# Performance work log

Hardware: AMD Instinct MI355X
Metric: run time of the kernel (lower is better)

Reference implementation:

```python
import jax, jax.numpy as jnp
import numpy as np

N = 50000
E = 800000
D_IN = 128
H = 256
L = 3


def setup_inputs() -> dict:
    key = jax.random.key(0)
    ks = jax.random.split(key, 12)
    x = jax.random.normal(ks[0], (N, D_IN), dtype=jnp.float32)
    edge_index = jax.random.randint(ks[1], (2, E), 0, N, dtype=jnp.int32)
    edge_attr = jax.random.uniform(ks[2], (E, 4), dtype=jnp.float32)
    s_enc = 1.0 / np.sqrt(D_IN)
    s_h = 1.0 / np.sqrt(H)
    W_enc = jax.random.uniform(ks[3], (D_IN, H), minval=-s_enc, maxval=s_enc)
    b_enc = jax.random.uniform(ks[4], (H,), minval=-s_enc, maxval=s_enc)
    W_g = jax.random.uniform(ks[5], (L, H, H), minval=-s_h, maxval=s_h)
    b_g = jax.random.uniform(ks[6], (L, H), minval=-s_h, maxval=s_h)
    W_out = jax.random.uniform(ks[7], (H, H), minval=-s_h, maxval=s_h)
    b_out = jax.random.uniform(ks[8], (H,), minval=-s_h, maxval=s_h)
    return {"x": x, "edge_index": edge_index, "edge_attr": edge_attr,
            "W_enc": W_enc, "b_enc": b_enc, "W_g": W_g, "b_g": b_g,
            "W_out": W_out, "b_out": b_out}


def _gcn_norm(edge_index, n):
    # PyG GCNConv: add self-loops, symmetric normalization D^-1/2 (A+I) D^-1/2
    loops = jnp.arange(n, dtype=edge_index.dtype)
    src = jnp.concatenate([edge_index[0], loops])  # [E+N]
    dst = jnp.concatenate([edge_index[1], loops])  # [E+N]
    deg = jax.ops.segment_sum(jnp.ones_like(dst, dtype=jnp.float32), dst, num_segments=n)
    dinv = jnp.where(deg > 0, jax.lax.rsqrt(deg), 0.0)
    norm = dinv[src] * dinv[dst]  # [E+N]
    return src, dst, norm


def _gcn_conv(h, W, b, src, dst, norm, n):
    m = h @ W                                  # [N,H] transform first
    agg = jax.ops.segment_sum(m[src] * norm[:, None], dst, num_segments=n)
    return agg + b


def reference(x, edge_index, edge_attr, W_enc, b_enc, W_g, b_g, W_out, b_out):
    n = x.shape[0]
    src, dst, norm = _gcn_norm(edge_index, n)
    h = jax.nn.relu(x @ W_enc + b_enc)
    for i in range(W_g.shape[0]):
        h = jax.nn.relu(_gcn_conv(h, W_g[i], b_g[i], src, dst, norm, n))
        # dropout is identity in eval mode
    return h @ W_out + b_out
```

## Files before the change

kernel.cpp:

```cpp
#include <hip/hip_runtime.h>
#include <math.h>

#define N_NODES 50000
#define N_EDGES 800000
#define D_IN    128
#define H_DIM   256
#define L_LAYERS 3
#define SCAN_BLOCKS ((N_NODES + 255) / 256)

typedef _Float16 f16x8 __attribute__((ext_vector_type(8)));
typedef _Float16 f16x4 __attribute__((ext_vector_type(4)));
typedef float    f32x4 __attribute__((ext_vector_type(4)));


__global__ __launch_bounds__(256) void zero_kernel(int* __restrict__ counts,
                                                   int* __restrict__ cursor, int n) {
    int i = blockIdx.x * 256 + threadIdx.x;
    if (i < n) { counts[i] = 0; cursor[i] = 0; }
}

__global__ __launch_bounds__(256) void hist_kernel(const int* __restrict__ dst,
                                                   int* __restrict__ counts, int e_cnt) {
    int e = blockIdx.x * 256 + threadIdx.x;
    if (e < e_cnt) atomicAdd(&counts[dst[e]], 1);
}

__global__ __launch_bounds__(256) void scanA_kernel(const int* __restrict__ counts,
                                                    int* __restrict__ blocksum,
                                                    float* __restrict__ dinv, int n) {
    __shared__ int s[256];
    int t = threadIdx.x;
    int i = blockIdx.x * 256 + t;
    int v = (i < n) ? counts[i] : 0;
    if (i < n) dinv[i] = rsqrtf((float)(v + 1));
    s[t] = v;
    __syncthreads();
#pragma unroll
    for (int d = 128; d > 0; d >>= 1) {
        if (t < d) s[t] += s[t + d];
        __syncthreads();
    }
    if (t == 0) blocksum[blockIdx.x] = s[0];
}

__global__ __launch_bounds__(256) void scanB_kernel(int* __restrict__ blocksum,
                                                    int* __restrict__ offsets,
                                                    int nblocks, int n, int total) {
    __shared__ int s[256];
    int t = threadIdx.x;
    int v = (t < nblocks) ? blocksum[t] : 0;
    s[t] = v;
    __syncthreads();
#pragma unroll
    for (int d = 1; d < 256; d <<= 1) {
        int x = (t >= d) ? s[t - d] : 0;
        __syncthreads();
        s[t] += x;
        __syncthreads();
    }
    if (t < nblocks) blocksum[t] = s[t] - v;
    if (t == 0) offsets[n] = total;
}

__global__ __launch_bounds__(256) void scanC_kernel(const int* __restrict__ counts,
                                                    const int* __restrict__ blocksum,
                                                    int* __restrict__ offsets, int n) {
    __shared__ int s[256];
    int t = threadIdx.x;
    int i = blockIdx.x * 256 + t;
    int v = (i < n) ? counts[i] : 0;
    s[t] = v;
    __syncthreads();
#pragma unroll
    for (int d = 1; d < 256; d <<= 1) {
        int x = (t >= d) ? s[t - d] : 0;
        __syncthreads();
        s[t] += x;
        __syncthreads();
    }
    if (i < n) offsets[i] = blocksum[blockIdx.x] + s[t] - v;
}

__global__ __launch_bounds__(256) void fill_kernel(const int* __restrict__ src,
                                                   const int* __restrict__ dst,
                                                   const int* __restrict__ offsets,
                                                   int* __restrict__ cursor,
                                                   const float* __restrict__ dinv,
                                                   int* __restrict__ csr_src,
                                                   float* __restrict__ csr_w, int e_cnt) {
    int e = blockIdx.x * 256 + threadIdx.x;
    if (e < e_cnt) {
        int d = dst[e];
        int pos = offsets[d] + atomicAdd(&cursor[d], 1);
        int s = src[e];
        csr_src[pos] = s;
        csr_w[pos]   = dinv[s];
    }
}


__global__ __launch_bounds__(256) void aggregate_kernel(const _Float16* __restrict__ h,
                                                        const int* __restrict__ offsets,
                                                        const int* __restrict__ csr_src,
                                                        const float* __restrict__ csr_w,
                                                        const float* __restrict__ dinv,
                                                        _Float16* __restrict__ outp, int n) {
    int wave = threadIdx.x >> 6;
    int lane = threadIdx.x & 63;
    int v = blockIdx.x * 4 + wave;
    if (v >= n) return;
    int c = lane * 4;
    float dv = dinv[v];
    f16x4 self = *(const f16x4*)(h + (size_t)v * H_DIM + c);
    float ax = dv * (float)self[0];
    float ay = dv * (float)self[1];
    float az = dv * (float)self[2];
    float aw = dv * (float)self[3];

    int e  = offsets[v];
    int e1 = offsets[v + 1];
    for (; e + 3 < e1; e += 4) {
        int   s0 = csr_src[e],     s1 = csr_src[e + 1];
        int   s2 = csr_src[e + 2], s3 = csr_src[e + 3];
        float w0 = csr_w[e],       w1 = csr_w[e + 1];
        float w2 = csr_w[e + 2],   w3 = csr_w[e + 3];
        f16x4 a = *(const f16x4*)(h + (size_t)s0 * H_DIM + c);
        f16x4 b = *(const f16x4*)(h + (size_t)s1 * H_DIM + c);
        f16x4 d = *(const f16x4*)(h + (size_t)s2 * H_DIM + c);
        f16x4 f = *(const f16x4*)(h + (size_t)s3 * H_DIM + c);
        ax += w0 * (float)a[0] + w1 * (float)b[0] + w2 * (float)d[0] + w3 * (float)f[0];
        ay += w0 * (float)a[1] + w1 * (float)b[1] + w2 * (float)d[1] + w3 * (float)f[1];
        az += w0 * (float)a[2] + w1 * (float)b[2] + w2 * (float)d[2] + w3 * (float)f[2];
        aw += w0 * (float)a[3] + w1 * (float)b[3] + w2 * (float)d[3] + w3 * (float)f[3];
    }
    for (; e < e1; ++e) {
        int   s0 = csr_src[e];
        float w0 = csr_w[e];
        f16x4 a = *(const f16x4*)(h + (size_t)s0 * H_DIM + c);
        ax += w0 * (float)a[0]; ay += w0 * (float)a[1];
        az += w0 * (float)a[2]; aw += w0 * (float)a[3];
    }
    f16x4 o;
    o[0] = (_Float16)(ax * dv);
    o[1] = (_Float16)(ay * dv);
    o[2] = (_Float16)(az * dv);
    o[3] = (_Float16)(aw * dv);
    *(f16x4*)(outp + (size_t)v * H_DIM + c) = o;
}


#define WCONV_TOTAL 294912

__global__ __launch_bounds__(256) void wconv_kernel(const float* __restrict__ W_enc,
                                                    const float* __restrict__ W_g,
                                                    const float* __restrict__ W_out,
                                                    _Float16* __restrict__ whi,
                                                    _Float16* __restrict__ wlo) {
    int gid = blockIdx.x * 256 + threadIdx.x;
    if (gid >= WCONV_TOTAL) return;
    const float* src; int base, e;
    if (gid < 32768)       { src = W_enc; base = 0;      e = gid; }
    else if (gid < 229376) { src = W_g;   base = 32768;  e = gid - 32768; }
    else                   { src = W_out; base = 229376; e = gid - 229376; }
    int k = e >> 8;
    int n = e & 255;
    float x = src[e];
    _Float16 hb = (_Float16)x;
    _Float16 lb = (_Float16)(x - (float)hb);
    int dst = base + (k >> 5) * 8192 + (n >> 4) * 512 + ((k & 31) >> 3) * 128
            + (n & 15) * 8 + (k & 7);
    whi[dst] = hb;
    wlo[dst] = lb;
}


template <int AMODE, int OUT16>
__global__ __launch_bounds__(256, 3) void mfma_gemm(const float* __restrict__ Af,
                                                    const _Float16* __restrict__ A16,
                                                    int K,
                                                    const _Float16* __restrict__ WhG,
                                                    const _Float16* __restrict__ WlG,
                                                    const float* __restrict__ bias,
                                                    float* __restrict__ Cf,
                                                    _Float16* __restrict__ Ch,
                                                    int n, int relu) {
    __shared__ _Float16 Wh[8192];
    __shared__ _Float16 Wl[8192];

    int t = threadIdx.x;
    int w = t >> 6;
    int lane = t & 63;
    int row0 = blockIdx.x * 64;
    int mrow = lane & 15;
    int koct = (lane >> 4) * 8;

    f32x4 acc[4][4];
#pragma unroll
    for (int mt = 0; mt < 4; ++mt)
#pragma unroll
        for (int c = 0; c < 4; ++c)
            acc[mt][c] = (f32x4)(0.0f);

    int rows[4];
#pragma unroll
    for (int mt = 0; mt < 4; ++mt) {
        int r = row0 + mt * 16 + mrow;
        rows[mt] = (r < n) ? r : (n - 1);
    }

    int nkc = K >> 5;
    for (int kc = 0; kc < nkc; ++kc) {
        {
            const _Float16* gh = WhG + (size_t)kc * 8192;
            const _Float16* gl = WlG + (size_t)kc * 8192;
#pragma unroll
            for (int i = 0; i < 4; ++i) {
                int chunk = w * 4 + i;
                __builtin_amdgcn_global_load_lds(
                    (const __attribute__((address_space(1))) unsigned int*)(gh + chunk * 512 + lane * 8),
                    (__attribute__((address_space(3))) unsigned int*)(&Wh[chunk * 512]),
                    16, 0, 0);
                __builtin_amdgcn_global_load_lds(
                    (const __attribute__((address_space(1))) unsigned int*)(gl + chunk * 512 + lane * 8),
                    (__attribute__((address_space(3))) unsigned int*)(&Wl[chunk * 512]),
                    16, 0, 0);
            }
        }

        f16x8 ahf[4], alf[4];
        if (AMODE == 1) {
#pragma unroll
            for (int mt = 0; mt < 4; ++mt)
                ahf[mt] = *(const f16x8*)(A16 + (size_t)rows[mt] * K + kc * 32 + koct);
        } else {
#pragma unroll
            for (int mt = 0; mt < 4; ++mt) {
                const float* p = Af + (size_t)rows[mt] * K + kc * 32 + koct;
                float4 a0 = *(const float4*)p;
                float4 a1 = *(const float4*)(p + 4);
                float xs[8] = {a0.x, a0.y, a0.z, a0.w, a1.x, a1.y, a1.z, a1.w};
                f16x8 H, L;
#pragma unroll
                for (int j = 0; j < 8; ++j) {
                    _Float16 hb = (_Float16)xs[j];
                    H[j] = hb;
                    L[j] = (_Float16)(xs[j] - (float)hb);
                }
                ahf[mt] = H;
                alf[mt] = L;
            }
        }
        __syncthreads();

#pragma unroll
        for (int c = 0; c < 4; ++c) {
            int nt = w * 4 + c;
            f16x8 bh = *(const f16x8*)&Wh[(nt * 64 + lane) * 8];
            f16x8 bl = *(const f16x8*)&Wl[(nt * 64 + lane) * 8];
#pragma unroll
            for (int mt = 0; mt < 4; ++mt) {
                acc[mt][c] = __builtin_amdgcn_mfma_f32_16x16x32_f16(ahf[mt], bh, acc[mt][c], 0, 0, 0);
                acc[mt][c] = __builtin_amdgcn_mfma_f32_16x16x32_f16(ahf[mt], bl, acc[mt][c], 0, 0, 0);
                if (AMODE == 0)
                    acc[mt][c] = __builtin_amdgcn_mfma_f32_16x16x32_f16(alf[mt], bh, acc[mt][c], 0, 0, 0);
            }
        }
        __syncthreads();
    }

    int colq = lane & 15;
    int rowq = (lane >> 4) * 4;
#pragma unroll
    for (int c = 0; c < 4; ++c) {
        int col = w * 64 + c * 16 + colq;
        float b = bias[col];
#pragma unroll
        for (int mt = 0; mt < 4; ++mt) {
            int rb = row0 + mt * 16 + rowq;
#pragma unroll
            for (int r = 0; r < 4; ++r) {
                int row = rb + r;
                if (row < n) {
                    float v = acc[mt][c][r] + b;
                    if (relu) v = fmaxf(v, 0.f);
                    if (OUT16) Ch[(size_t)row * H_DIM + col] = (_Float16)v;
                    else       Cf[(size_t)row * H_DIM + col] = v;
                }
            }
        }
    }
}


extern "C" void kernel_launch(void* const* d_in, const int* in_sizes, int n_in,
                              void* d_out, int out_size, void* d_ws, size_t ws_size,
                              hipStream_t stream) {
    const float* x     = (const float*)d_in[0];
    const int*   ei    = (const int*)d_in[1];
    const float* W_enc = (const float*)d_in[3];
    const float* b_enc = (const float*)d_in[4];
    const float* W_g   = (const float*)d_in[5];
    const float* b_g   = (const float*)d_in[6];
    const float* W_out = (const float*)d_in[7];
    const float* b_out = (const float*)d_in[8];
    float* out = (float*)d_out;

    char* ws = (char*)d_ws;
    size_t off = 0;
    auto alloc = [&](size_t bytes) -> void* {
        void* p = ws + off;
        off = (off + bytes + 255) & ~(size_t)255;
        return p;
    };
    int*       counts   = (int*)alloc((size_t)N_NODES * 4);
    int*       offsets  = (int*)alloc((size_t)(N_NODES + 1) * 4);
    int*       cursor   = (int*)alloc((size_t)N_NODES * 4);
    float*     dinv     = (float*)alloc((size_t)N_NODES * 4);
    int*       blocksum = (int*)alloc((size_t)SCAN_BLOCKS * 4);
    int*       csr_src  = (int*)alloc((size_t)N_EDGES * 4);
    float*     csr_w    = (float*)alloc((size_t)N_EDGES * 4);
    _Float16*  h16      = (_Float16*)alloc((size_t)N_NODES * H_DIM * 2);
    _Float16*  agg16    = (_Float16*)alloc((size_t)N_NODES * H_DIM * 2);
    _Float16*  whi      = (_Float16*)alloc((size_t)WCONV_TOTAL * 2);
    _Float16*  wlo      = (_Float16*)alloc((size_t)WCONV_TOTAL * 2);

    const int* src = ei;
    const int* dst = ei + N_EDGES;

    zero_kernel<<<(N_NODES + 255) / 256, 256, 0, stream>>>(counts, cursor, N_NODES);
    hist_kernel<<<(N_EDGES + 255) / 256, 256, 0, stream>>>(dst, counts, N_EDGES);
    scanA_kernel<<<SCAN_BLOCKS, 256, 0, stream>>>(counts, blocksum, dinv, N_NODES);
    scanB_kernel<<<1, 256, 0, stream>>>(blocksum, offsets, SCAN_BLOCKS, N_NODES, N_EDGES);
    scanC_kernel<<<SCAN_BLOCKS, 256, 0, stream>>>(counts, blocksum, offsets, N_NODES);
    fill_kernel<<<(N_EDGES + 255) / 256, 256, 0, stream>>>(src, dst, offsets, cursor, dinv,
                                                           csr_src, csr_w, N_EDGES);
    wconv_kernel<<<(WCONV_TOTAL + 255) / 256, 256, 0, stream>>>(W_enc, W_g, W_out, whi, wlo);

    int gemm_grid = (N_NODES + 63) / 64;
    mfma_gemm<0, 1><<<gemm_grid, 256, 0, stream>>>(x, (const _Float16*)nullptr, D_IN,
                                                   whi, wlo, b_enc,
                                                   (float*)nullptr, h16, N_NODES, 1);
    for (int l = 0; l < L_LAYERS; ++l) {
        aggregate_kernel<<<N_NODES / 4, 256, 0, stream>>>(h16, offsets, csr_src, csr_w, dinv,
                                                          agg16, N_NODES);
        mfma_gemm<1, 1><<<gemm_grid, 256, 0, stream>>>((const float*)nullptr, agg16, H_DIM,
                                                       whi + 32768 + (size_t)l * 65536,
                                                       wlo + 32768 + (size_t)l * 65536,
                                                       b_g + (size_t)l * H_DIM,
                                                       (float*)nullptr, h16, N_NODES, 1);
    }
    mfma_gemm<1, 0><<<gemm_grid, 256, 0, stream>>>((const float*)nullptr, h16, H_DIM,
                                                   whi + 229376, wlo + 229376, b_out,
                                                   out, (_Float16*)nullptr, N_NODES, 0);
}
```

Baseline: 563.7 us.

## Make GEMM persistent with resident weight column slices and software-prefetched A tiles

The GEMM becomes a persistent kernel of 512 blocks. Each block loads a 64-column slice of the full-K weights into LDS once, then loops over 256-row tiles, prefetching the next K-chunk of A into registers while the current one runs through MFMA. This removes the per-K-chunk weight reloads and barriers and hides A load latency, at the cost of lower occupancy (launch bounds 2) and extra register pressure. The aggregation loop is also widened to batch 8 neighbor gathers per iteration, giving more memory-level parallelism.

```diff
diff --git a/kernel.cpp b/kernel.cpp
--- a/kernel.cpp
+++ b/kernel.cpp
@@ -119,21 +119,48 @@
 
     int e  = offsets[v];
     int e1 = offsets[v + 1];
-    for (; e + 3 < e1; e += 4) {
-        int   s0 = csr_src[e],     s1 = csr_src[e + 1];
-        int   s2 = csr_src[e + 2], s3 = csr_src[e + 3];
-        float w0 = csr_w[e],       w1 = csr_w[e + 1];
-        float w2 = csr_w[e + 2],   w3 = csr_w[e + 3];
+
+    for (; e + 7 < e1; e += 8) {
+        int   s_[8]; float w_[8]; f16x4 r_[8];
+#pragma unroll
+        for (int j = 0; j < 8; ++j) { s_[j] = csr_src[e + j]; w_[j] = csr_w[e + j]; }
+#pragma unroll
+        for (int j = 0; j < 8; ++j) r_[j] = *(const f16x4*)(h + (size_t)s_[j] * H_DIM + c);
+#pragma unroll
+        for (int j = 0; j < 8; ++j) {
+            ax += w_[j] * (float)r_[j][0];
+            ay += w_[j] * (float)r_[j][1];
+            az += w_[j] * (float)r_[j][2];
+            aw += w_[j] * (float)r_[j][3];
+        }
+    }
+    if (e + 3 < e1) {
+        int   s_[4]; float w_[4]; f16x4 r_[4];
+#pragma unroll
+        for (int j = 0; j < 4; ++j) { s_[j] = csr_src[e + j]; w_[j] = csr_w[e + j]; }
+#pragma unroll
+        for (int j = 0; j < 4; ++j) r_[j] = *(const f16x4*)(h + (size_t)s_[j] * H_DIM + c);
+#pragma unroll
+        for (int j = 0; j < 4; ++j) {
+            ax += w_[j] * (float)r_[j][0];
+            ay += w_[j] * (float)r_[j][1];
+            az += w_[j] * (float)r_[j][2];
+            aw += w_[j] * (float)r_[j][3];
+        }
+        e += 4;
+    }
+    if (e + 1 < e1) {
+        int   s0 = csr_src[e],  s1 = csr_src[e + 1];
+        float w0 = csr_w[e],    w1 = csr_w[e + 1];
         f16x4 a = *(const f16x4*)(h + (size_t)s0 * H_DIM + c);
         f16x4 b = *(const f16x4*)(h + (size_t)s1 * H_DIM + c);
-        f16x4 d = *(const f16x4*)(h + (size_t)s2 * H_DIM + c);
-        f16x4 f = *(const f16x4*)(h + (size_t)s3 * H_DIM + c);
-        ax += w0 * (float)a[0] + w1 * (float)b[0] + w2 * (float)d[0] + w3 * (float)f[0];
-        ay += w0 * (float)a[1] + w1 * (float)b[1] + w2 * (float)d[1] + w3 * (float)f[1];
-        az += w0 * (float)a[2] + w1 * (float)b[2] + w2 * (float)d[2] + w3 * (float)f[2];
-        aw += w0 * (float)a[3] + w1 * (float)b[3] + w2 * (float)d[3] + w3 * (float)f[3];
-    }
-    for (; e < e1; ++e) {
+        ax += w0 * (float)a[0] + w1 * (float)b[0];
+        ay += w0 * (float)a[1] + w1 * (float)b[1];
+        az += w0 * (float)a[2] + w1 * (float)b[2];
+        aw += w0 * (float)a[3] + w1 * (float)b[3];
+        e += 2;
+    }
+    if (e < e1) {
         int   s0 = csr_src[e];
         float w0 = csr_w[e];
         f16x4 a = *(const f16x4*)(h + (size_t)s0 * H_DIM + c);
@@ -174,117 +201,153 @@
 }
 
 
-template <int AMODE, int OUT16>
-__global__ __launch_bounds__(256, 3) void mfma_gemm(const float* __restrict__ Af,
+template <int KC, int AMODE, int OUT16>
+__global__ __launch_bounds__(256, 2) void mfma_gemm(const float* __restrict__ Af,
                                                     const _Float16* __restrict__ A16,
-                                                    int K,
                                                     const _Float16* __restrict__ WhG,
                                                     const _Float16* __restrict__ WlG,
                                                     const float* __restrict__ bias,
                                                     float* __restrict__ Cf,
                                                     _Float16* __restrict__ Ch,
                                                     int n, int relu) {
-    __shared__ _Float16 Wh[8192];
-    __shared__ _Float16 Wl[8192];
+    constexpr int K = KC * 32;
+    __shared__ _Float16 Wh[KC * 2048];
+    __shared__ _Float16 Wl[KC * 2048];
 
     int t = threadIdx.x;
     int w = t >> 6;
     int lane = t & 63;
-    int row0 = blockIdx.x * 64;
+    int q = blockIdx.x & 3;
+    int colbase = q * 64;
     int mrow = lane & 15;
     int koct = (lane >> 4) * 8;
 
-    f32x4 acc[4][4];
-#pragma unroll
-    for (int mt = 0; mt < 4; ++mt)
-#pragma unroll
-        for (int c = 0; c < 4; ++c)
-            acc[mt][c] = (f32x4)(0.0f);
-
-    int rows[4];
-#pragma unroll
-    for (int mt = 0; mt < 4; ++mt) {
-        int r = row0 + mt * 16 + mrow;
-        rows[mt] = (r < n) ? r : (n - 1);
-    }
-
-    int nkc = K >> 5;
-    for (int kc = 0; kc < nkc; ++kc) {
-        {
-            const _Float16* gh = WhG + (size_t)kc * 8192;
-            const _Float16* gl = WlG + (size_t)kc * 8192;
-#pragma unroll
-            for (int i = 0; i < 4; ++i) {
-                int chunk = w * 4 + i;
-                __builtin_amdgcn_global_load_lds(
-                    (const __attribute__((address_space(1))) unsigned int*)(gh + chunk * 512 + lane * 8),
-                    (__attribute__((address_space(3))) unsigned int*)(&Wh[chunk * 512]),
-                    16, 0, 0);
-                __builtin_amdgcn_global_load_lds(
-                    (const __attribute__((address_space(1))) unsigned int*)(gl + chunk * 512 + lane * 8),
-                    (__attribute__((address_space(3))) unsigned int*)(&Wl[chunk * 512]),
-                    16, 0, 0);
-            }
-        }
-
-        f16x8 ahf[4], alf[4];
-        if (AMODE == 1) {
-#pragma unroll
-            for (int mt = 0; mt < 4; ++mt)
-                ahf[mt] = *(const f16x8*)(A16 + (size_t)rows[mt] * K + kc * 32 + koct);
-        } else {
-#pragma unroll
-            for (int mt = 0; mt < 4; ++mt) {
-                const float* p = Af + (size_t)rows[mt] * K + kc * 32 + koct;
-                float4 a0 = *(const float4*)p;
-                float4 a1 = *(const float4*)(p + 4);
-                float xs[8] = {a0.x, a0.y, a0.z, a0.w, a1.x, a1.y, a1.z, a1.w};
-                f16x8 H, L;
-#pragma unroll
-                for (int j = 0; j < 8; ++j) {
-                    _Float16 hb = (_Float16)xs[j];
-                    H[j] = hb;
-                    L[j] = (_Float16)(xs[j] - (float)hb);
-                }
-                ahf[mt] = H;
-                alf[mt] = L;
-            }
-        }
-        __syncthreads();
-
-#pragma unroll
-        for (int c = 0; c < 4; ++c) {
-            int nt = w * 4 + c;
-            f16x8 bh = *(const f16x8*)&Wh[(nt * 64 + lane) * 8];
-            f16x8 bl = *(const f16x8*)&Wl[(nt * 64 + lane) * 8];
-#pragma unroll
-            for (int mt = 0; mt < 4; ++mt) {
-                acc[mt][c] = __builtin_amdgcn_mfma_f32_16x16x32_f16(ahf[mt], bh, acc[mt][c], 0, 0, 0);
-                acc[mt][c] = __builtin_amdgcn_mfma_f32_16x16x32_f16(ahf[mt], bl, acc[mt][c], 0, 0, 0);
-                if (AMODE == 0)
-                    acc[mt][c] = __builtin_amdgcn_mfma_f32_16x16x32_f16(alf[mt], bh, acc[mt][c], 0, 0, 0);
-            }
-        }
-        __syncthreads();
-    }
+#pragma unroll
+    for (int kc = 0; kc < KC; ++kc) {
+        __builtin_amdgcn_global_load_lds(
+            (const __attribute__((address_space(1))) unsigned int*)(WhG + kc * 8192 + q * 2048 + t * 8),
+            (__attribute__((address_space(3))) unsigned int*)(&Wh[kc * 2048 + t * 8]), 16, 0, 0);
+        __builtin_amdgcn_global_load_lds(
+            (const __attribute__((address_space(1))) unsigned int*)(WlG + kc * 8192 + q * 2048 + t * 8),
+            (__attribute__((address_space(3))) unsigned int*)(&Wl[kc * 2048 + t * 8]), 16, 0, 0);
+    }
+    __syncthreads();
 
     int colq = lane & 15;
     int rowq = (lane >> 4) * 4;
-#pragma unroll
-    for (int c = 0; c < 4; ++c) {
-        int col = w * 64 + c * 16 + colq;
-        float b = bias[col];
+    float bcol[4];
+#pragma unroll
+    for (int c = 0; c < 4; ++c) bcol[c] = bias[colbase + c * 16 + colq];
+
+    for (int rt = blockIdx.x >> 2; rt * 256 < n; rt += 128) {
+        int rbase = rt * 256 + w * 64;
+        int rows[4];
 #pragma unroll
         for (int mt = 0; mt < 4; ++mt) {
-            int rb = row0 + mt * 16 + rowq;
-#pragma unroll
-            for (int r = 0; r < 4; ++r) {
-                int row = rb + r;
-                if (row < n) {
-                    float v = acc[mt][c][r] + b;
-                    if (relu) v = fmaxf(v, 0.f);
-                    if (OUT16) Ch[(size_t)row * H_DIM + col] = (_Float16)v;
-                    else       Cf[(size_t)row * H_DIM + col] = v;
+            int r = rbase + mt * 16 + mrow;
+            rows[mt] = (r < n) ? r : (n - 1);
+        }
+
+        f32x4 acc[4][4];
+#pragma unroll
+        for (int mt = 0; mt < 4; ++mt)
+#pragma unroll
+            for (int c = 0; c < 4; ++c)
+                acc[mt][c] = (f32x4)(0.0f);
+
+        f16x8 a16c[4], a16n[4];
+        float4 af0c[4], af1c[4], af0n[4], af1n[4];
+        if (AMODE == 1) {
+#pragma unroll
+            for (int mt = 0; mt < 4; ++mt)
+                a16c[mt] = *(const f16x8*)(A16 + (size_t)rows[mt] * K + koct);
+        } else {
+#pragma unroll
+            for (int mt = 0; mt < 4; ++mt) {
+                const float* p = Af + (size_t)rows[mt] * K + koct;
+                af0c[mt] = *(const float4*)p;
+                af1c[mt] = *(const float4*)(p + 4);
+            }
+        }
+
+#pragma unroll
+        for (int kc = 0; kc < KC; ++kc) {
+            if (kc + 1 < KC) {
+                if (AMODE == 1) {
+#pragma unroll
+                    for (int mt = 0; mt < 4; ++mt)
+                        a16n[mt] = *(const f16x8*)(A16 + (size_t)rows[mt] * K + (kc + 1) * 32 + koct);
+                } else {
+#pragma unroll
+                    for (int mt = 0; mt < 4; ++mt) {
+                        const float* p = Af + (size_t)rows[mt] * K + (kc + 1) * 32 + koct;
+                        af0n[mt] = *(const float4*)p;
+                        af1n[mt] = *(const float4*)(p + 4);
+                    }
+                }
+            }
+
+            f16x8 ah[4], al[4];
+            if (AMODE == 1) {
+#pragma unroll
+                for (int mt = 0; mt < 4; ++mt) ah[mt] = a16c[mt];
+            } else {
+#pragma unroll
+                for (int mt = 0; mt < 4; ++mt) {
+                    float xs[8] = {af0c[mt].x, af0c[mt].y, af0c[mt].z, af0c[mt].w,
+                                   af1c[mt].x, af1c[mt].y, af1c[mt].z, af1c[mt].w};
+                    f16x8 H, L;
+#pragma unroll
+                    for (int j = 0; j < 8; ++j) {
+                        _Float16 hb = (_Float16)xs[j];
+                        H[j] = hb;
+                        L[j] = (_Float16)(xs[j] - (float)hb);
+                    }
+                    ah[mt] = H;
+                    al[mt] = L;
+                }
+            }
+
+#pragma unroll
+            for (int c = 0; c < 4; ++c) {
+                f16x8 bh = *(const f16x8*)&Wh[kc * 2048 + c * 512 + lane * 8];
+                f16x8 bl = *(const f16x8*)&Wl[kc * 2048 + c * 512 + lane * 8];
+#pragma unroll
+                for (int mt = 0; mt < 4; ++mt) {
+                    acc[mt][c] = __builtin_amdgcn_mfma_f32_16x16x32_f16(ah[mt], bh, acc[mt][c], 0, 0, 0);
+                    acc[mt][c] = __builtin_amdgcn_mfma_f32_16x16x32_f16(ah[mt], bl, acc[mt][c], 0, 0, 0);
+                    if (AMODE == 0)
+                        acc[mt][c] = __builtin_amdgcn_mfma_f32_16x16x32_f16(al[mt], bh, acc[mt][c], 0, 0, 0);
+                }
+            }
+
+            if (AMODE == 1) {
+#pragma unroll
+                for (int mt = 0; mt < 4; ++mt) a16c[mt] = a16n[mt];
+            } else {
+#pragma unroll
+                for (int mt = 0; mt < 4; ++mt) {
+                    af0c[mt] = af0n[mt];
+                    af1c[mt] = af1n[mt];
+                }
+            }
+        }
+
+#pragma unroll
+        for (int c = 0; c < 4; ++c) {
+            int col = colbase + c * 16 + colq;
+#pragma unroll
+            for (int mt = 0; mt < 4; ++mt) {
+                int rb = rbase + mt * 16 + rowq;
+#pragma unroll
+                for (int r = 0; r < 4; ++r) {
+                    int row = rb + r;
+                    if (row < n) {
+                        float v = acc[mt][c][r] + bcol[c];
+                        if (relu) v = fmaxf(v, 0.f);
+                        if (OUT16) Ch[(size_t)row * H_DIM + col] = (_Float16)v;
+                        else       Cf[(size_t)row * H_DIM + col] = v;
+                    }
                 }
             }
         }
@@ -336,20 +399,19 @@
                                                            csr_src, csr_w, N_EDGES);
     wconv_kernel<<<(WCONV_TOTAL + 255) / 256, 256, 0, stream>>>(W_enc, W_g, W_out, whi, wlo);
 
-    int gemm_grid = (N_NODES + 63) / 64;
-    mfma_gemm<0, 1><<<gemm_grid, 256, 0, stream>>>(x, (const _Float16*)nullptr, D_IN,
-                                                   whi, wlo, b_enc,
-                                                   (float*)nullptr, h16, N_NODES, 1);
+    mfma_gemm<4, 0, 1><<<512, 256, 0, stream>>>(x, (const _Float16*)nullptr,
+                                                whi, wlo, b_enc,
+                                                (float*)nullptr, h16, N_NODES, 1);
     for (int l = 0; l < L_LAYERS; ++l) {
         aggregate_kernel<<<N_NODES / 4, 256, 0, stream>>>(h16, offsets, csr_src, csr_w, dinv,
                                                           agg16, N_NODES);
-        mfma_gemm<1, 1><<<gemm_grid, 256, 0, stream>>>((const float*)nullptr, agg16, H_DIM,
-                                                       whi + 32768 + (size_t)l * 65536,
-                                                       wlo + 32768 + (size_t)l * 65536,
-                                                       b_g + (size_t)l * H_DIM,
-                                                       (float*)nullptr, h16, N_NODES, 1);
-    }
-    mfma_gemm<1, 0><<<gemm_grid, 256, 0, stream>>>((const float*)nullptr, h16, H_DIM,
-                                                   whi + 229376, wlo + 229376, b_out,
-                                                   out, (_Float16*)nullptr, N_NODES, 0);
-}
+        mfma_gemm<8, 1, 1><<<512, 256, 0, stream>>>((const float*)nullptr, agg16,
+                                                    whi + 32768 + (size_t)l * 65536,
+                                                    wlo + 32768 + (size_t)l * 65536,
+                                                    b_g + (size_t)l * H_DIM,
+                                                    (float*)nullptr, h16, N_NODES, 1);
+    }
+    mfma_gemm<8, 1, 0><<<512, 256, 0, stream>>>((const float*)nullptr, h16,
+                                                whi + 229376, wlo + 229376, b_out,
+                                                out, (_Float16*)nullptr, N_NODES, 0);
+}
```

Measured after the change: 641.1 us. 1.14x slower.
